# Optimization experiments

Hardware: AMD Instinct MI355X
Metric: run time of the kernel (lower is better)

The kernel has to match this reference:

```python
import jax, jax.numpy as jnp
import numpy as np

N = 100000
E = 1600000
F_IN = 128
F_HID = 64


def setup_inputs() -> dict:
    key = jax.random.key(0)
    ks = jax.random.split(key, 8)
    x = jax.random.normal(ks[0], (N, F_IN), dtype=jnp.float32)
    edge_index = jax.random.randint(ks[1], (2, E), 0, N, dtype=jnp.int64)
    # GCNConv params (PyG default: weight, then bias added after aggregation)
    s1 = 1.0 / np.sqrt(F_IN)
    s2 = 1.0 / np.sqrt(F_HID)
    W1 = jax.random.uniform(ks[2], (F_IN, F_HID), jnp.float32, -s1, s1)
    b1 = jnp.zeros((F_HID,), jnp.float32)
    W2 = jax.random.uniform(ks[3], (F_HID, F_HID), jnp.float32, -s2, s2)
    b2 = jnp.zeros((F_HID,), jnp.float32)
    # Linear(hidden, 1) for predict_link
    Wout = jax.random.uniform(ks[4], (F_HID, 1), jnp.float32, -s2, s2)
    bout = jax.random.uniform(ks[5], (1,), jnp.float32, -s2, s2)
    return {"x": x, "edge_index": edge_index, "W1": W1, "b1": b1,
            "W2": W2, "b2": b2, "Wout": Wout, "bout": bout}


def _gcn_conv(x, row, col, W, b):
    # x: [N, Fin]; row/col: [E'] (self-loops already appended)
    h = x @ W                                              # [N, Fout]
    deg = jax.ops.segment_sum(jnp.ones_like(col, dtype=h.dtype), col,
                              num_segments=N)              # [N]
    dinv = jnp.where(deg > 0, jax.lax.rsqrt(jnp.maximum(deg, 1e-12)), 0.0)
    norm = dinv[row] * dinv[col]                           # [E']
    msg = h[row] * norm[:, None]                           # [E', Fout]
    out = jax.ops.segment_sum(msg, col, num_segments=N)    # [N, Fout]
    return out + b


def reference(x, edge_index, W1, b1, W2, b2, Wout, bout):
    row0, col0 = edge_index[0], edge_index[1]
    # add self-loops (GCNConv default)
    loop = jnp.arange(N, dtype=edge_index.dtype)
    row = jnp.concatenate([row0, loop])
    col = jnp.concatenate([col0, loop])

    h = jax.nn.relu(_gcn_conv(x, row, col, W1, b1))   # dropout p=0.0 (eval)
    h = jax.nn.relu(_gcn_conv(h, row, col, W2, b2))

    # predict_link on the original (no-self-loop) edges
    edge_features = h[row0] * h[col0]                 # [E, F_HID]
    return edge_features @ Wout + bout                # [E, 1]
```

## Files before the change

kernel.cpp:

```cpp
#include <hip/hip_runtime.h>

#define NN 100000
#define EE 1600000
#define FIN 128
#define FHID 64

#define BSH 7
#define NB  ((NN + 127) / 128)
#define CAP 3072
#define BIN_BLOCKS 256
#define BIN_EPT 8
#define BIN_EPB (1024 * BIN_EPT)

typedef union { _Float16 h[4]; uint2 u; } H4;
typedef union { _Float16 h[8]; uint4 u; } H8;

__global__ void k_zero_int(int* __restrict__ p, int n) {
    int i = blockIdx.x * blockDim.x + threadIdx.x;
    if (i < n) p[i] = 0;
}

__global__ __launch_bounds__(1024) void k_bin(const int* __restrict__ row,
                                              const int* __restrict__ col,
                                              int* __restrict__ bcnt,
                                              unsigned long long* __restrict__ rec) {
    __shared__ int hist[NB];
    __shared__ int base[NB];
    int tid = threadIdx.x;
    for (int i = tid; i < NB; i += 1024) hist[i] = 0;
    __syncthreads();
    int e0 = blockIdx.x * BIN_EPB;
    int b[BIN_EPT];
    int rnk[BIN_EPT];
    unsigned long long pk[BIN_EPT];
#pragma unroll
    for (int j = 0; j < BIN_EPT; ++j) {
        int e = e0 + j * 1024 + tid;
        b[j] = -1;
        if (e < EE) {
            int c = col[e];
            int r = row[e];
            b[j] = c >> BSH;
            pk[j] = ((unsigned long long)(unsigned)c << 17) | (unsigned)r;
            rnk[j] = atomicAdd(&hist[b[j]], 1);
        }
    }
    __syncthreads();
    for (int i = tid; i < NB; i += 1024) {
        int h = hist[i];
        base[i] = h ? atomicAdd(&bcnt[i], h) : 0;
    }
    __syncthreads();
#pragma unroll
    for (int j = 0; j < BIN_EPT; ++j) {
        if (b[j] >= 0) {
            int p = base[b[j]] + rnk[j];
            if (p < CAP) rec[(size_t)b[j] * CAP + p] = pk[j];
        }
    }
}

__global__ __launch_bounds__(256) void k_csr(const int* __restrict__ bcnt,
                                             const unsigned long long* __restrict__ rec,
                                             int* __restrict__ csr_src,
                                             int* __restrict__ starts,
                                             int* __restrict__ degi,
                                             float* __restrict__ dinv) {
    __shared__ unsigned short rank[CAP];
    __shared__ int nh[128];
    __shared__ int ns[128];
    __shared__ int nsx[128];
    int b = blockIdx.x;
    int tid = threadIdx.x;
    int cnt = bcnt[b];
    if (cnt > CAP) cnt = CAP;
    int gb = b * CAP;
    const unsigned long long* r = rec + (size_t)b * CAP;
    if (tid < 128) nh[tid] = 0;
    __syncthreads();
    for (int i = tid; i < cnt; i += 256) {
        int c = (int)(r[i] >> 17);
        int cl = c - (b << BSH);
        rank[i] = (unsigned short)atomicAdd(&nh[cl], 1);
    }
    __syncthreads();
    if (tid < 128) ns[tid] = nh[tid];
    __syncthreads();
    for (int off = 1; off < 128; off <<= 1) {
        int x = 0;
        if (tid < 128 && tid >= off) x = ns[tid - off];
        __syncthreads();
        if (tid < 128) ns[tid] += x;
        __syncthreads();
    }
    if (tid < 128) {
        int excl = ns[tid] - nh[tid];
        nsx[tid] = excl;
        int n = (b << BSH) + tid;
        if (n < NN) {
            starts[n] = gb + excl;
            degi[n] = nh[tid];
            dinv[n] = rsqrtf((float)(nh[tid] + 1));
        }
    }
    __syncthreads();
    for (int i = tid; i < cnt; i += 256) {
        unsigned long long rv = r[i];
        int c = (int)(rv >> 17);
        int cl = c - (b << BSH);
        csr_src[gb + nsx[cl] + (int)rank[i]] = (int)(rv & 0x1FFFF);
    }
}

#define XPAD 129
__global__ __launch_bounds__(512) void k_gemm1(const float* __restrict__ x,
                                               const float* __restrict__ W1,
                                               const float* __restrict__ dinv,
                                               uint4* __restrict__ hs16) {
    __shared__ float xl[64 * XPAD];
    int tid = threadIdx.x;
    int n0 = blockIdx.x * 64;
    const float4* x4 = reinterpret_cast<const float4*>(x);
#pragma unroll
    for (int i = 0; i < 4; ++i) {
        int idx = i * 512 + tid;
        int row = idx >> 5;
        int k4 = idx & 31;
        float4 v = {0.f, 0.f, 0.f, 0.f};
        if (n0 + row < NN) v = x4[(size_t)(n0 + row) * 32 + k4];
        float* p = &xl[row * XPAD + k4];
        p[0] = v.x; p[32] = v.y; p[64] = v.z; p[96] = v.w;
    }
    __syncthreads();

    int wv = __builtin_amdgcn_readfirstlane(tid >> 6);
    int lane = tid & 63;
    float acc[8];
#pragma unroll
    for (int c = 0; c < 8; ++c) acc[c] = 0.f;
    const float* Wb = W1 + wv * 8;
    const float* xrow = &xl[lane * XPAD];
#pragma unroll 8
    for (int k = 0; k < FIN; ++k) {
        float xk = xrow[((k & 3) << 5) | (k >> 2)];
        const float* wr = Wb + k * FHID;
#pragma unroll
        for (int c = 0; c < 8; ++c) acc[c] = fmaf(xk, wr[c], acc[c]);
    }

    int node = n0 + lane;
    if (node < NN) {
        float dn = dinv[node];
        H8 pk;
#pragma unroll
        for (int c = 0; c < 8; ++c) pk.h[c] = (_Float16)(acc[c] * dn);
        hs16[(size_t)node * 8 + wv] = pk.u;
    }
}

#define X2PAD 65
typedef union { _Float16 h[16]; uint4 u[2]; } H16;
__global__ __launch_bounds__(256) void k_gemm2(const uint2* __restrict__ y1,
                                               const float* __restrict__ W2,
                                               const float* __restrict__ dinv,
                                               uint4* __restrict__ hs16) {
    __shared__ float al[64 * X2PAD];
    int tid = threadIdx.x;
    int n0 = blockIdx.x * 64;
#pragma unroll
    for (int i = 0; i < 4; ++i) {
        int idx = i * 256 + tid;
        int rw = idx >> 4;
        int k4 = idx & 15;
        float4 v = {0.f, 0.f, 0.f, 0.f};
        if (n0 + rw < NN) {
            H4 t;
            t.u = y1[(size_t)(n0 + rw) * 16 + k4];
            v.x = (float)t.h[0]; v.y = (float)t.h[1];
            v.z = (float)t.h[2]; v.w = (float)t.h[3];
        }
        float* p = &al[rw * X2PAD + k4];
        p[0] = v.x; p[16] = v.y; p[32] = v.z; p[48] = v.w;
    }
    __syncthreads();

    int wv = __builtin_amdgcn_readfirstlane(tid >> 6);
    int lane = tid & 63;
    float acc[16];
#pragma unroll
    for (int c = 0; c < 16; ++c) acc[c] = 0.f;
    const float* Wb = W2 + wv * 16;
    const float* arow = &al[lane * X2PAD];
#pragma unroll 8
    for (int k = 0; k < FHID; ++k) {
        float xk = arow[((k & 3) << 4) | (k >> 2)];
        const float* wr = Wb + k * FHID;
#pragma unroll
        for (int c = 0; c < 16; ++c) acc[c] = fmaf(xk, wr[c], acc[c]);
    }

    int node = n0 + lane;
    if (node < NN) {
        float dn = dinv[node];
        H16 pk;
#pragma unroll
        for (int c = 0; c < 16; ++c) pk.h[c] = (_Float16)(acc[c] * dn);
        hs16[(size_t)node * 8 + wv * 2] = pk.u[0];
        hs16[(size_t)node * 8 + wv * 2 + 1] = pk.u[1];
    }
}

__global__ __launch_bounds__(256) void k_gath(const int* __restrict__ starts,
                                              const int* __restrict__ degi,
                                              const int* __restrict__ csr_src,
                                              const float* __restrict__ dinv,
                                              const uint4* __restrict__ hIn,
                                              const float* __restrict__ bias,
                                              uint4* __restrict__ yOut) {
    int wave = threadIdx.x >> 6;
    int lane = threadIdx.x & 63;
    int g = lane >> 3;
    int fl = lane & 7;
    int n = blockIdx.x * 4 + wave;
    if (n >= NN) return;
    int s = starts[n];
    int d = degi[n];
    int idx = (lane < d) ? csr_src[s + lane] : 0;
    float a[8];
    H8 pk;
    if (g == 0) {
        pk.u = hIn[(size_t)n * 8 + fl];
#pragma unroll
        for (int j = 0; j < 8; ++j) a[j] = (float)pk.h[j];
    } else {
#pragma unroll
        for (int j = 0; j < 8; ++j) a[j] = 0.f;
    }
    int dc = d < 64 ? d : 64;
    for (int k = g; k < dc; k += 8) {
        int r = __shfl(idx, k);
        H8 v;
        v.u = hIn[(size_t)r * 8 + fl];
#pragma unroll
        for (int j = 0; j < 8; ++j) a[j] += (float)v.h[j];
    }
    for (int k = 64 + g; k < d; k += 8) {
        int r = csr_src[s + k];
        H8 v;
        v.u = hIn[(size_t)r * 8 + fl];
#pragma unroll
        for (int j = 0; j < 8; ++j) a[j] += (float)v.h[j];
    }
#pragma unroll
    for (int j = 0; j < 8; ++j) {
        a[j] += __shfl_xor(a[j], 8);
        a[j] += __shfl_xor(a[j], 16);
        a[j] += __shfl_xor(a[j], 32);
    }
    if (g == 0) {
        float dn = dinv[n];
        float4 b0 = reinterpret_cast<const float4*>(bias)[fl * 2];
        float4 b1 = reinterpret_cast<const float4*>(bias)[fl * 2 + 1];
        H8 o;
        o.h[0] = (_Float16)fmaxf(fmaf(a[0], dn, b0.x), 0.f);
        o.h[1] = (_Float16)fmaxf(fmaf(a[1], dn, b0.y), 0.f);
        o.h[2] = (_Float16)fmaxf(fmaf(a[2], dn, b0.z), 0.f);
        o.h[3] = (_Float16)fmaxf(fmaf(a[3], dn, b0.w), 0.f);
        o.h[4] = (_Float16)fmaxf(fmaf(a[4], dn, b1.x), 0.f);
        o.h[5] = (_Float16)fmaxf(fmaf(a[5], dn, b1.y), 0.f);
        o.h[6] = (_Float16)fmaxf(fmaf(a[6], dn, b1.z), 0.f);
        o.h[7] = (_Float16)fmaxf(fmaf(a[7], dn, b1.w), 0.f);
        yOut[(size_t)n * 8 + fl] = o.u;
    }
}

__global__ __launch_bounds__(256) void k_link(const int* __restrict__ row0,
                                              const int* __restrict__ col0,
                                              const uint4* __restrict__ y16,
                                              const float* __restrict__ Wout,
                                              const float* __restrict__ bout,
                                              float* __restrict__ out) {
    int wid = blockIdx.x * 4 + (threadIdx.x >> 6);
    int lane = threadIdx.x & 63;
    int sub = lane >> 3;
    int fl = lane & 7;
    float4 w0 = reinterpret_cast<const float4*>(Wout)[fl * 2];
    float4 w1 = reinterpret_cast<const float4*>(Wout)[fl * 2 + 1];
    float wv[8] = {w0.x, w0.y, w0.z, w0.w, w1.x, w1.y, w1.z, w1.w};
    float bout0 = bout[0];
    const int NBATCH = EE / 64;
    int stride = gridDim.x * 4;
    for (int q = wid; q < NBATCH; q += stride) {
        int e0 = q * 64;
        int r64 = row0[e0 + lane];
        int c64 = col0[e0 + lane];
#pragma unroll
        for (int it = 0; it < 8; ++it) {
            int k = it * 8 + sub;
            int r = __shfl(r64, k);
            int c = __shfl(c64, k);
            H8 hr, hc;
            hr.u = y16[(size_t)r * 8 + fl];
            hc.u = y16[(size_t)c * 8 + fl];
            float p = 0.f;
#pragma unroll
            for (int j = 0; j < 8; ++j)
                p = fmaf((float)hr.h[j], (float)hc.h[j] * wv[j], p);
            p += __shfl_xor(p, 1);
            p += __shfl_xor(p, 2);
            p += __shfl_xor(p, 4);
            if (fl == 0) out[e0 + k] = p + bout0;
        }
    }
}

extern "C" void kernel_launch(void* const* d_in, const int* in_sizes, int n_in,
                              void* d_out, int out_size, void* d_ws, size_t ws_size,
                              hipStream_t stream) {
    const float* x    = (const float*)d_in[0];
    const int*   ei   = (const int*)d_in[1];
    const float* W1   = (const float*)d_in[2];
    const float* b1   = (const float*)d_in[3];
    const float* W2   = (const float*)d_in[4];
    const float* b2   = (const float*)d_in[5];
    const float* Wout = (const float*)d_in[6];
    const float* bout = (const float*)d_in[7];
    const int*   row0 = ei;
    const int*   col0 = ei + EE;

    char* ws = (char*)d_ws;
    auto align = [](size_t v) { return (v + 255) / 256 * 256; };
    const size_t nInt = align((size_t)NN * 4);
    float* dinv    = (float*)ws;                 ws += nInt;
    int*   degi    = (int*)ws;                   ws += nInt;
    int*   starts  = (int*)ws;                   ws += nInt;
    int*   bcnt    = (int*)ws;                   ws += align((size_t)NB * 4);
    int*   csr_src = (int*)ws;                   ws += align((size_t)NB * CAP * 4);
    uint4* bufH    = (uint4*)ws;                 ws += align((size_t)NN * FHID * 2);
    uint4* bufY    = (uint4*)ws;                 ws += align((size_t)NN * FHID * 2);
    unsigned long long* rec = (unsigned long long*)bufH;
    float* out = (float*)d_out;

    const int nTiles = (NN + 63) / 64;

    k_zero_int<<<(NB + 255) / 256, 256, 0, stream>>>(bcnt, NB);
    k_bin<<<BIN_BLOCKS, 1024, 0, stream>>>(row0, col0, bcnt, rec);
    k_csr<<<NB, 256, 0, stream>>>(bcnt, rec, csr_src, starts, degi, dinv);

    k_gemm1<<<nTiles, 512, 0, stream>>>(x, W1, dinv, bufH);
    k_gath<<<(NN + 3) / 4, 256, 0, stream>>>(starts, degi, csr_src, dinv, bufH, b1, bufY);

    k_gemm2<<<nTiles, 256, 0, stream>>>((const uint2*)bufY, W2, dinv, bufH);
    k_gath<<<(NN + 3) / 4, 256, 0, stream>>>(starts, degi, csr_src, dinv, bufH, b2, bufY);

    k_link<<<2048, 256, 0, stream>>>(row0, col0, bufY, Wout, bout, out);
}
```

Baseline: 216.1 us.

## Map one node per 8-lane group in gather and batch neighbor loads

The aggregation kernel now gives each node to one 8-lane group, so a wave handles 8 nodes instead of one. Each group preloads up to 24 neighbor indices in registers and fetches neighbors in unrolled chunks of 8 loads, which keeps more memory requests in flight. This removes the cross-group shuffle reduction and the idle lanes that appeared when a node had far fewer than 64 neighbors. The separate zeroing kernel is replaced with hipMemsetAsync. The cost is per-group divergence on degree and a serial tail loop for high-degree nodes.

```diff
diff --git a/kernel.cpp b/kernel.cpp
--- a/kernel.cpp
+++ b/kernel.cpp
@@ -14,11 +14,6 @@
 
 typedef union { _Float16 h[4]; uint2 u; } H4;
 typedef union { _Float16 h[8]; uint4 u; } H8;
-
-__global__ void k_zero_int(int* __restrict__ p, int n) {
-    int i = blockIdx.x * blockDim.x + threadIdx.x;
-    if (i < n) p[i] = 0;
-}
 
 __global__ __launch_bounds__(1024) void k_bin(const int* __restrict__ row,
                                               const int* __restrict__ col,
@@ -210,6 +205,25 @@
     }
 }
 
+#define GCHUNK8(IDXREG)                                                     \
+    {                                                                       \
+        H8 v0, v1, v2, v3, v4, v5, v6, v7;                                  \
+        v0.u = hIn[(size_t)__shfl(IDXREG, base + 0) * 8 + fl];              \
+        v1.u = hIn[(size_t)__shfl(IDXREG, base + 1) * 8 + fl];              \
+        v2.u = hIn[(size_t)__shfl(IDXREG, base + 2) * 8 + fl];              \
+        v3.u = hIn[(size_t)__shfl(IDXREG, base + 3) * 8 + fl];              \
+        v4.u = hIn[(size_t)__shfl(IDXREG, base + 4) * 8 + fl];              \
+        v5.u = hIn[(size_t)__shfl(IDXREG, base + 5) * 8 + fl];              \
+        v6.u = hIn[(size_t)__shfl(IDXREG, base + 6) * 8 + fl];              \
+        v7.u = hIn[(size_t)__shfl(IDXREG, base + 7) * 8 + fl];              \
+        _Pragma("unroll")                                                   \
+        for (int j = 0; j < 8; ++j)                                         \
+            a[j] += ((float)v0.h[j] + (float)v1.h[j]) +                     \
+                    ((float)v2.h[j] + (float)v3.h[j]) +                     \
+                    ((float)v4.h[j] + (float)v5.h[j]) +                     \
+                    ((float)v6.h[j] + (float)v7.h[j]);                      \
+    }
+
 __global__ __launch_bounds__(256) void k_gath(const int* __restrict__ starts,
                                               const int* __restrict__ degi,
                                               const int* __restrict__ csr_src,
@@ -221,57 +235,53 @@
     int lane = threadIdx.x & 63;
     int g = lane >> 3;
     int fl = lane & 7;
-    int n = blockIdx.x * 4 + wave;
+    int base = lane & 56;
+    int n = blockIdx.x * 32 + wave * 8 + g;
     if (n >= NN) return;
     int s = starts[n];
     int d = degi[n];
-    int idx = (lane < d) ? csr_src[s + lane] : 0;
+    int ia = (fl < d)      ? csr_src[s + fl]      : 0;
+    int ib = (8 + fl < d)  ? csr_src[s + 8 + fl]  : 0;
+    int ic = (16 + fl < d) ? csr_src[s + 16 + fl] : 0;
     float a[8];
     H8 pk;
-    if (g == 0) {
-        pk.u = hIn[(size_t)n * 8 + fl];
-#pragma unroll
-        for (int j = 0; j < 8; ++j) a[j] = (float)pk.h[j];
-    } else {
-#pragma unroll
-        for (int j = 0; j < 8; ++j) a[j] = 0.f;
-    }
-    int dc = d < 64 ? d : 64;
-    for (int k = g; k < dc; k += 8) {
-        int r = __shfl(idx, k);
+    pk.u = hIn[(size_t)n * 8 + fl];
+#pragma unroll
+    for (int j = 0; j < 8; ++j) a[j] = (float)pk.h[j];
+
+    int k = 0;
+    if (d >= 8)  { GCHUNK8(ia); k = 8; }
+    if (d >= 16) { GCHUNK8(ib); k = 16; }
+    if (d >= 24) { GCHUNK8(ic); k = 24; }
+    int lim = d < 24 ? d : 24;
+    for (; k < lim; ++k) {
+        int k8 = k >> 3;
+        int src = (k8 == 0) ? ia : ((k8 == 1) ? ib : ic);
         H8 v;
-        v.u = hIn[(size_t)r * 8 + fl];
+        v.u = hIn[(size_t)__shfl(src, base + (k & 7)) * 8 + fl];
 #pragma unroll
         for (int j = 0; j < 8; ++j) a[j] += (float)v.h[j];
     }
-    for (int k = 64 + g; k < d; k += 8) {
-        int r = csr_src[s + k];
+    for (; k < d; ++k) {
         H8 v;
-        v.u = hIn[(size_t)r * 8 + fl];
+        v.u = hIn[(size_t)csr_src[s + k] * 8 + fl];
 #pragma unroll
         for (int j = 0; j < 8; ++j) a[j] += (float)v.h[j];
     }
-#pragma unroll
-    for (int j = 0; j < 8; ++j) {
-        a[j] += __shfl_xor(a[j], 8);
-        a[j] += __shfl_xor(a[j], 16);
-        a[j] += __shfl_xor(a[j], 32);
-    }
-    if (g == 0) {
-        float dn = dinv[n];
-        float4 b0 = reinterpret_cast<const float4*>(bias)[fl * 2];
-        float4 b1 = reinterpret_cast<const float4*>(bias)[fl * 2 + 1];
-        H8 o;
-        o.h[0] = (_Float16)fmaxf(fmaf(a[0], dn, b0.x), 0.f);
-        o.h[1] = (_Float16)fmaxf(fmaf(a[1], dn, b0.y), 0.f);
-        o.h[2] = (_Float16)fmaxf(fmaf(a[2], dn, b0.z), 0.f);
-        o.h[3] = (_Float16)fmaxf(fmaf(a[3], dn, b0.w), 0.f);
-        o.h[4] = (_Float16)fmaxf(fmaf(a[4], dn, b1.x), 0.f);
-        o.h[5] = (_Float16)fmaxf(fmaf(a[5], dn, b1.y), 0.f);
-        o.h[6] = (_Float16)fmaxf(fmaf(a[6], dn, b1.z), 0.f);
-        o.h[7] = (_Float16)fmaxf(fmaf(a[7], dn, b1.w), 0.f);
-        yOut[(size_t)n * 8 + fl] = o.u;
-    }
+
+    float dn = dinv[n];
+    float4 b0 = reinterpret_cast<const float4*>(bias)[fl * 2];
+    float4 b1 = reinterpret_cast<const float4*>(bias)[fl * 2 + 1];
+    H8 o;
+    o.h[0] = (_Float16)fmaxf(fmaf(a[0], dn, b0.x), 0.f);
+    o.h[1] = (_Float16)fmaxf(fmaf(a[1], dn, b0.y), 0.f);
+    o.h[2] = (_Float16)fmaxf(fmaf(a[2], dn, b0.z), 0.f);
+    o.h[3] = (_Float16)fmaxf(fmaf(a[3], dn, b0.w), 0.f);
+    o.h[4] = (_Float16)fmaxf(fmaf(a[4], dn, b1.x), 0.f);
+    o.h[5] = (_Float16)fmaxf(fmaf(a[5], dn, b1.y), 0.f);
+    o.h[6] = (_Float16)fmaxf(fmaf(a[6], dn, b1.z), 0.f);
+    o.h[7] = (_Float16)fmaxf(fmaf(a[7], dn, b1.w), 0.f);
+    yOut[(size_t)n * 8 + fl] = o.u;
 }
 
 __global__ __launch_bounds__(256) void k_link(const int* __restrict__ row0,
@@ -343,15 +353,15 @@
 
     const int nTiles = (NN + 63) / 64;
 
-    k_zero_int<<<(NB + 255) / 256, 256, 0, stream>>>(bcnt, NB);
+    hipMemsetAsync(bcnt, 0, (size_t)NB * 4, stream);
     k_bin<<<BIN_BLOCKS, 1024, 0, stream>>>(row0, col0, bcnt, rec);
     k_csr<<<NB, 256, 0, stream>>>(bcnt, rec, csr_src, starts, degi, dinv);
 
     k_gemm1<<<nTiles, 512, 0, stream>>>(x, W1, dinv, bufH);
-    k_gath<<<(NN + 3) / 4, 256, 0, stream>>>(starts, degi, csr_src, dinv, bufH, b1, bufY);
+    k_gath<<<(NN + 31) / 32, 256, 0, stream>>>(starts, degi, csr_src, dinv, bufH, b1, bufY);
 
     k_gemm2<<<nTiles, 256, 0, stream>>>((const uint2*)bufY, W2, dinv, bufH);
-    k_gath<<<(NN + 3) / 4, 256, 0, stream>>>(starts, degi, csr_src, dinv, bufH, b2, bufY);
+    k_gath<<<(NN + 31) / 32, 256, 0, stream>>>(starts, degi, csr_src, dinv, bufH, b2, bufY);
 
     k_link<<<2048, 256, 0, stream>>>(row0, col0, bufY, Wout, bout, out);
 }
```

Measured after the change: 202.4 us. 1.07x faster.
